# Kernel tuning notes

Hardware: AMD Instinct MI355X
Metric: run time of the kernel (lower is better)

The kernel has to match this reference:

```python
import jax, jax.numpy as jnp
import numpy as np

INTERP = 10  # gt contour interpolation factor (time=10 in source)
SMOOTH_L1_BETA = 1.0
LOSS_WEIGHT = 1.0


def interpolation(poly):
    # poly: [B, M, 2] -> [B, M*INTERP, 2]
    poly_roll = jnp.roll(poly, shift=1, axis=1)
    step = jnp.arange(INTERP, dtype=poly.dtype) / INTERP  # [INTERP]
    # [B, M, INTERP, 2]
    interp = (poly[:, :, None, :] * step[None, None, :, None]
              + poly_roll[:, :, None, :] * (1.0 - step)[None, None, :, None])
    B, M = poly.shape[0], poly.shape[1]
    return interp.reshape(B, M * INTERP, 2)


def compute_distance(pred, gt):
    # pred: [B, N, 2], gt: [B, M, 2] -> squared euclidean distance [B, M, N]
    # ||g - p||^2 = ||g||^2 + ||p||^2 - 2 g.p  (avoids materializing [B,M,N,2])
    g2 = jnp.sum(gt * gt, axis=-1)[:, :, None]    # [B, M, 1]
    p2 = jnp.sum(pred * pred, axis=-1)[:, None, :]  # [B, 1, N]
    gp = jnp.einsum('bmk,bnk->bmn', gt, pred)
    return g2 + p2 - 2.0 * gp


def smooth_l1(x, y):
    d = jnp.abs(x - y)
    return jnp.where(d < SMOOTH_L1_BETA, 0.5 * d * d / SMOOTH_L1_BETA, d - 0.5 * SMOOTH_L1_BETA)


def setup_inputs() -> dict:
    key = jax.random.key(0)
    k1, k2, k3, k4 = jax.random.split(key, 4)
    B, N, M = 1024, 128, 128
    ini_pred_poly = jax.random.normal(k1, (B, N, 2), dtype=jnp.float32)
    pred_poly = ini_pred_poly + 0.1 * jax.random.normal(k2, (B, N, 2), dtype=jnp.float32)
    gt_poly = jax.random.normal(k3, (B, M, 2), dtype=jnp.float32)
    keyPointsMask = (jax.random.uniform(k4, (B, M)) < 0.7).astype(jnp.float32)
    return {'ini_pred_poly': ini_pred_poly, 'pred_poly': pred_poly,
            'gt_poly': gt_poly, 'keyPointsMask': keyPointsMask}


def reference(ini_pred_poly, pred_poly, gt_poly, keyPointsMask):
    # --- lossPred2NearestGt ---
    gt_interp = interpolation(gt_poly)                       # [B, M*10, 2]
    d1 = compute_distance(ini_pred_poly, gt_interp)          # [B, M*10, N]
    index_gt = jnp.argmin(d1, axis=1)                        # [B, N]
    nearest_gt = jnp.take_along_axis(gt_interp, index_gt[:, :, None], axis=1)  # [B, N, 2]
    loss_pred2gt = jnp.mean(smooth_l1(pred_poly, nearest_gt))  # scalar (reduction='mean')

    # --- lossGt2NearestPred ---
    d2 = compute_distance(ini_pred_poly, gt_poly)            # [B, M, N]
    index_pred = jnp.argmin(d2, axis=2)                      # [B, M]
    nearest_pred = jnp.take_along_axis(pred_poly, index_pred[:, :, None], axis=1)  # [B, M, 2]
    loss_gt2pred = smooth_l1(nearest_pred, gt_poly)          # [B, M, 2] (reduction='none')

    # mask expanded to [B, M, 2] in the source -> its sum counts both coords
    mask = keyPointsMask[:, :, None]
    masked_sum = jnp.sum(loss_gt2pred * mask)
    mask_sum = 2.0 * jnp.sum(keyPointsMask)
    loss_set2set = masked_sum / (mask_sum + 1.0) + loss_pred2gt
    loss = loss_set2set / 2.0
    return LOSS_WEIGHT * loss
```

## Files before the change

### kernel.cpp

```cpp
#include <hip/hip_runtime.h>
#include <math.h>


#define BB 1024
#define NN 128
#define MM 128

__device__ __forceinline__ float sl1(float x) {
    float d = fabsf(x);
    return d < 1.0f ? 0.5f * d * d : d - 0.5f;
}

__global__ void __launch_bounds__(256, 8)
dmloss_main(const float* __restrict__ ini, const float* __restrict__ pred,
            const float* __restrict__ gt,  const float* __restrict__ kmask,
            float4* __restrict__ partials)
{
    const int b    = blockIdx.x >> 1;
    const int half = blockIdx.x & 1;
    const int tid  = threadIdx.x;
    const int g    = tid & 63;
    const int h    = tid >> 6;
    const int P    = (half << 6) + g;

    __shared__ __align__(16) float2 s_gt[MM];
    __shared__ float2 s_pr[NN];
    __shared__ float2 s_ii[NN];
    __shared__ float4 s_segA[MM];
    __shared__ float2 s_segB[MM];
    __shared__ float  s_step[16];
    __shared__ float  s_rv[4 * 64];
    __shared__ float  s_rf[4 * 64];
    __shared__ float  s_sum[3][4];

    const float2* gt2 = (const float2*)(gt   + (size_t)b * MM * 2);
    const float2* in2 = (const float2*)(ini  + (size_t)b * NN * 2);
    const float2* pr2 = (const float2*)(pred + (size_t)b * NN * 2);

    if (tid < 128) {
        int m = tid;
        float2 gm = gt2[m];
        float2 a  = gt2[(m + 127) & 127];
        s_gt[m] = gm;
        float ex = gm.x - a.x, ey = gm.y - a.y;
        float A  = ex * ex + ey * ey;
        float inv = A > 0.f ? 10.f / A : 0.f;
        s_segA[m] = make_float4(a.x, a.y, -ex * inv, -ey * inv);
        s_segB[m] = make_float2(ex * 0.1f, ey * 0.1f);
        if (tid < 16) s_step[tid] = (float)tid / 10.0f;
    } else {
        int k = tid - 128;
        s_pr[k] = pr2[k];
        s_ii[k] = in2[k];
    }
    float2 myP  = in2[P];
    float2 myPr = pr2[P];
    float2 myG  = gt2[P];
    float  myKm = kmask[b * MM + P];
    const float px = myP.x, py = myP.y;
    __syncthreads();

    float sumA = 0.f, sumB = 0.f, sumC = 0.f;

    float b0 = INFINITY, f0 = 1e30f;
    {
        float fm = (float)(320 * h);
        const int m0 = 32 * h;
        #pragma unroll 4
        for (int j = 0; j < 32; ++j) {
            float4 SA = s_segA[m0 + j];
            float2 SB = s_segB[m0 + j];
            float qx = SA.x - px, qy = SA.y - py;
            float jv = fmaf(qy, SA.w, qx * SA.z);
            float jr = rintf(__builtin_amdgcn_fmed3f(jv, 0.f, 9.f));
            float dx = fmaf(jr, SB.x, qx);
            float dy = fmaf(jr, SB.y, qy);
            float d  = fmaf(dy, dy, dx * dx);
            float fi = fm + jr;
            if (d < b0) { b0 = d; f0 = fi; }
            fm += 10.f;
        }
    }
    s_rv[h * 64 + g] = b0;
    s_rf[h * 64 + g] = f0;
    __syncthreads();

    if (tid < 64) {
        float best = s_rv[tid], bf = s_rf[tid];
        #pragma unroll
        for (int q = 1; q < 4; ++q) {
            float ov = s_rv[q * 64 + tid];
            float of = s_rf[q * 64 + tid];
            if (ov < best || (ov == best && of < bf)) { best = ov; bf = of; }
        }
        int bidx = (int)bf;
        int m = bidx / 10;
        int j = bidx - m * 10;
        float s  = s_step[j];
        float tt = 1.0f - s;
        float2 gm = s_gt[m];
        float2 gp = s_gt[(m + 127) & 127];
        float gx = gm.x * s + gp.x * tt;
        float gy = gm.y * s + gp.y * tt;
        float2 pr = s_pr[(half << 6) + tid];
        sumA = sl1(pr.x - gx) + sl1(pr.y - gy);
    }
    __syncthreads();

    {
        const float gx = myG.x, gy = myG.y;
        b0 = INFINITY; f0 = 1e30f;
        float fk = (float)(32 * h);
        const int k0 = 32 * h;
        #pragma unroll 4
        for (int j = 0; j < 32; ++j) {
            float2 I = s_ii[k0 + j];
            float dx = I.x - gx, dy = I.y - gy;
            float d  = fmaf(dy, dy, dx * dx);
            if (d < b0) { b0 = d; f0 = fk; }
            fk += 1.f;
        }
        s_rv[h * 64 + g] = b0;
        s_rf[h * 64 + g] = f0;
    }
    __syncthreads();

    if (tid < 64) {
        float best = s_rv[tid], bf = s_rf[tid];
        #pragma unroll
        for (int q = 1; q < 4; ++q) {
            float ov = s_rv[q * 64 + tid];
            float of = s_rf[q * 64 + tid];
            if (ov < best || (ov == best && of < bf)) { best = ov; bf = of; }
        }
        int k = (int)bf;
        float2 pk2 = s_pr[k];
        float2 g0  = s_gt[(half << 6) + tid];
        float  km  = kmask[b * MM + (half << 6) + tid];
        sumB = km * (sl1(pk2.x - g0.x) + sl1(pk2.y - g0.y));
        sumC = km;
    }

    #pragma unroll
    for (int off = 32; off > 0; off >>= 1) {
        sumA += __shfl_down(sumA, off);
        sumB += __shfl_down(sumB, off);
        sumC += __shfl_down(sumC, off);
    }
    const int wave = tid >> 6;
    if ((tid & 63) == 0) {
        s_sum[0][wave] = sumA; s_sum[1][wave] = sumB; s_sum[2][wave] = sumC;
    }
    __syncthreads();
    if (tid == 0) {
        float A = 0.f, Bs = 0.f, C = 0.f;
        #pragma unroll
        for (int w = 0; w < 4; ++w) {
            A += s_sum[0][w]; Bs += s_sum[1][w]; C += s_sum[2][w];
        }
        partials[blockIdx.x] = make_float4(A, Bs, C, 0.0f);
    }
}

__global__ void __launch_bounds__(256)
dmloss_final(const float4* __restrict__ partials, float* __restrict__ out)
{
    const int tid = threadIdx.x;
    float A = 0.0f, Bs = 0.0f, C = 0.0f;
    #pragma unroll
    for (int i = tid; i < 2 * BB; i += 256) {
        float4 p = partials[i];
        A += p.x; Bs += p.y; C += p.z;
    }
    #pragma unroll
    for (int off = 32; off > 0; off >>= 1) {
        A  += __shfl_down(A, off);
        Bs += __shfl_down(Bs, off);
        C  += __shfl_down(C, off);
    }
    __shared__ float sA[4], sB[4], sC[4];
    const int wave = tid >> 6, lane = tid & 63;
    if (lane == 0) { sA[wave] = A; sB[wave] = Bs; sC[wave] = C; }
    __syncthreads();
    if (tid == 0) {
        float a  = sA[0] + sA[1] + sA[2] + sA[3];
        float bs = sB[0] + sB[1] + sB[2] + sB[3];
        float c  = sC[0] + sC[1] + sC[2] + sC[3];
        float loss_pred2gt = a / ((float)BB * (float)NN * 2.0f);
        float loss_set2set = bs / (2.0f * c + 1.0f) + loss_pred2gt;
        out[0] = 0.5f * loss_set2set;
    }
}

extern "C" void kernel_launch(void* const* d_in, const int* in_sizes, int n_in,
                              void* d_out, int out_size, void* d_ws, size_t ws_size,
                              hipStream_t stream)
{
    const float* ini   = (const float*)d_in[0];
    const float* pred  = (const float*)d_in[1];
    const float* gt    = (const float*)d_in[2];
    const float* kmask = (const float*)d_in[3];
    float4* partials = (float4*)d_ws;

    dmloss_main<<<dim3(2 * BB), dim3(256), 0, stream>>>(ini, pred, gt, kmask, partials);
    dmloss_final<<<dim3(1), dim3(256), 0, stream>>>(partials, (float*)d_out);
}
```

Measured before the change: 18.08 us.

## Replace cross-wave argmin reduction with DPP row-rotation and per-wave role split

Each block now runs 128 threads. One wave computes the pred-to-gt nearest search and the other computes the gt-to-pred search. Query points and running (distance,index) minima are rotated across 16-lane rows with DPP row_ror, so each lane scans segments held by its row neighbours. This removes the shared-memory partial-min arrays and several block barriers. In exchange it adds per-step DPP moves and 64-bit packed compares, and halves threads per block.

```diff
diff --git a/kernel.cpp b/kernel.cpp
--- a/kernel.cpp
+++ b/kernel.cpp
@@ -6,38 +6,50 @@
 #define NN 128
 #define MM 128
 
+typedef unsigned long long u64;
+typedef unsigned int u32;
+
 __device__ __forceinline__ float sl1(float x) {
     float d = fabsf(x);
     return d < 1.0f ? 0.5f * d * d : d - 0.5f;
 }
 
-__global__ void __launch_bounds__(256, 8)
+__device__ __forceinline__ float dpp_ror1_f(float v) {
+    return __builtin_bit_cast(float,
+        __builtin_amdgcn_mov_dpp(__builtin_bit_cast(int, v), 0x121, 0xf, 0xf, false));
+}
+__device__ __forceinline__ u32 dpp_ror1_u(u32 v) {
+    return (u32)__builtin_amdgcn_mov_dpp((int)v, 0x121, 0xf, 0xf, false);
+}
+
+__global__ void __launch_bounds__(128, 8)
 dmloss_main(const float* __restrict__ ini, const float* __restrict__ pred,
             const float* __restrict__ gt,  const float* __restrict__ kmask,
             float4* __restrict__ partials)
 {
-    const int b    = blockIdx.x >> 1;
-    const int half = blockIdx.x & 1;
+    const int bid  = blockIdx.x;
+    const int b    = bid >> 1;
+    const int half = bid & 1;
     const int tid  = threadIdx.x;
-    const int g    = tid & 63;
-    const int h    = tid >> 6;
-    const int P    = (half << 6) + g;
+    const int wid  = tid >> 6;
+    const int lane = tid & 63;
+    const int lr   = lane & 15;
+    const int role = wid ^ half;
+    const int P    = (half << 6) + lane;
 
-    __shared__ __align__(16) float2 s_gt[MM];
+    __shared__ float2 s_gt[MM];
+    __shared__ float4 s_segA[MM];
+    __shared__ float2 s_segB[MM];
     __shared__ float2 s_pr[NN];
     __shared__ float2 s_ii[NN];
-    __shared__ float4 s_segA[MM];
-    __shared__ float2 s_segB[MM];
     __shared__ float  s_step[16];
-    __shared__ float  s_rv[4 * 64];
-    __shared__ float  s_rf[4 * 64];
-    __shared__ float  s_sum[3][4];
+    __shared__ float  s_sum[3][2];
 
     const float2* gt2 = (const float2*)(gt   + (size_t)b * MM * 2);
     const float2* in2 = (const float2*)(ini  + (size_t)b * NN * 2);
     const float2* pr2 = (const float2*)(pred + (size_t)b * NN * 2);
 
-    if (tid < 128) {
+    {
         int m = tid;
         float2 gm = gt2[m];
         float2 a  = gt2[(m + 127) & 127];
@@ -47,98 +59,78 @@
         float inv = A > 0.f ? 10.f / A : 0.f;
         s_segA[m] = make_float4(a.x, a.y, -ex * inv, -ey * inv);
         s_segB[m] = make_float2(ex * 0.1f, ey * 0.1f);
+        s_ii[m] = in2[m];
+        s_pr[m] = pr2[m];
         if (tid < 16) s_step[tid] = (float)tid / 10.0f;
-    } else {
-        int k = tid - 128;
-        s_pr[k] = pr2[k];
-        s_ii[k] = in2[k];
     }
     float2 myP  = in2[P];
     float2 myPr = pr2[P];
     float2 myG  = gt2[P];
     float  myKm = kmask[b * MM + P];
-    const float px = myP.x, py = myP.y;
     __syncthreads();
 
     float sumA = 0.f, sumB = 0.f, sumC = 0.f;
 
-    float b0 = INFINITY, f0 = 1e30f;
-    {
-        float fm = (float)(320 * h);
-        const int m0 = 32 * h;
-        #pragma unroll 4
-        for (int j = 0; j < 32; ++j) {
-            float4 SA = s_segA[m0 + j];
-            float2 SB = s_segB[m0 + j];
-            float qx = SA.x - px, qy = SA.y - py;
-            float jv = fmaf(qy, SA.w, qx * SA.z);
-            float jr = rintf(__builtin_amdgcn_fmed3f(jv, 0.f, 9.f));
-            float dx = fmaf(jr, SB.x, qx);
-            float dy = fmaf(jr, SB.y, qy);
-            float d  = fmaf(dy, dy, dx * dx);
-            float fi = fm + jr;
-            if (d < b0) { b0 = d; f0 = fi; }
-            fm += 10.f;
+    if (role == 0) {
+        float px = myP.x, py = myP.y;
+        u64 best = 0x7F800000FFFFFFFFull;
+        #pragma unroll 2
+        for (int g = 0; g < 8; ++g) {
+            float4 SA = s_segA[16 * g + lr];
+            float2 SB = s_segB[16 * g + lr];
+            float base = (float)(10 * (16 * g + lr));
+            #pragma unroll
+            for (int t = 0; t < 16; ++t) {
+                float qx = SA.x - px, qy = SA.y - py;
+                float jv = fmaf(qy, SA.w, qx * SA.z);
+                float jr = rintf(__builtin_amdgcn_fmed3f(jv, 0.f, 9.f));
+                float dx = fmaf(jr, SB.x, qx);
+                float dy = fmaf(jr, SB.y, qy);
+                float d  = fmaf(dy, dy, dx * dx);
+                u64 c = ((u64)__builtin_bit_cast(u32, d) << 32)
+                        | (u32)(base + jr);
+                best = c < best ? c : best;
+                px = dpp_ror1_f(px);
+                py = dpp_ror1_f(py);
+                u32 bl = dpp_ror1_u((u32)best);
+                u32 bh = dpp_ror1_u((u32)(best >> 32));
+                best = ((u64)bh << 32) | bl;
+            }
         }
-    }
-    s_rv[h * 64 + g] = b0;
-    s_rf[h * 64 + g] = f0;
-    __syncthreads();
-
-    if (tid < 64) {
-        float best = s_rv[tid], bf = s_rf[tid];
-        #pragma unroll
-        for (int q = 1; q < 4; ++q) {
-            float ov = s_rv[q * 64 + tid];
-            float of = s_rf[q * 64 + tid];
-            if (ov < best || (ov == best && of < bf)) { best = ov; bf = of; }
-        }
-        int bidx = (int)bf;
-        int m = bidx / 10;
-        int j = bidx - m * 10;
+        u32 idx = (u32)best;
+        int m = (int)idx / 10;
+        int j = (int)idx - 10 * m;
         float s  = s_step[j];
         float tt = 1.0f - s;
         float2 gm = s_gt[m];
         float2 gp = s_gt[(m + 127) & 127];
         float gx = gm.x * s + gp.x * tt;
         float gy = gm.y * s + gp.y * tt;
-        float2 pr = s_pr[(half << 6) + tid];
-        sumA = sl1(pr.x - gx) + sl1(pr.y - gy);
-    }
-    __syncthreads();
-
-    {
-        const float gx = myG.x, gy = myG.y;
-        b0 = INFINITY; f0 = 1e30f;
-        float fk = (float)(32 * h);
-        const int k0 = 32 * h;
-        #pragma unroll 4
-        for (int j = 0; j < 32; ++j) {
-            float2 I = s_ii[k0 + j];
-            float dx = I.x - gx, dy = I.y - gy;
-            float d  = fmaf(dy, dy, dx * dx);
-            if (d < b0) { b0 = d; f0 = fk; }
-            fk += 1.f;
+        sumA = sl1(myPr.x - gx) + sl1(myPr.y - gy);
+    } else {
+        float gx = myG.x, gy = myG.y;
+        u64 best = 0x7F800000FFFFFFFFull;
+        #pragma unroll 2
+        for (int g = 0; g < 8; ++g) {
+            float2 I = s_ii[16 * g + lr];
+            const u32 lo = (u32)(16 * g + lr);
+            #pragma unroll
+            for (int t = 0; t < 16; ++t) {
+                float dx = I.x - gx, dy = I.y - gy;
+                float d  = fmaf(dy, dy, dx * dx);
+                u64 c = ((u64)__builtin_bit_cast(u32, d) << 32) | lo;
+                best = c < best ? c : best;
+                gx = dpp_ror1_f(gx);
+                gy = dpp_ror1_f(gy);
+                u32 bl = dpp_ror1_u((u32)best);
+                u32 bh = dpp_ror1_u((u32)(best >> 32));
+                best = ((u64)bh << 32) | bl;
+            }
         }
-        s_rv[h * 64 + g] = b0;
-        s_rf[h * 64 + g] = f0;
-    }
-    __syncthreads();
-
-    if (tid < 64) {
-        float best = s_rv[tid], bf = s_rf[tid];
-        #pragma unroll
-        for (int q = 1; q < 4; ++q) {
-            float ov = s_rv[q * 64 + tid];
-            float of = s_rf[q * 64 + tid];
-            if (ov < best || (ov == best && of < bf)) { best = ov; bf = of; }
-        }
-        int k = (int)bf;
-        float2 pk2 = s_pr[k];
-        float2 g0  = s_gt[(half << 6) + tid];
-        float  km  = kmask[b * MM + (half << 6) + tid];
-        sumB = km * (sl1(pk2.x - g0.x) + sl1(pk2.y - g0.y));
-        sumC = km;
+        u32 k = (u32)best;
+        float2 pk = s_pr[k];
+        sumB = myKm * (sl1(pk.x - myG.x) + sl1(pk.y - myG.y));
+        sumC = myKm;
     }
 
     #pragma unroll
@@ -147,18 +139,14 @@
         sumB += __shfl_down(sumB, off);
         sumC += __shfl_down(sumC, off);
     }
-    const int wave = tid >> 6;
-    if ((tid & 63) == 0) {
-        s_sum[0][wave] = sumA; s_sum[1][wave] = sumB; s_sum[2][wave] = sumC;
+    if (lane == 0) {
+        s_sum[0][wid] = sumA; s_sum[1][wid] = sumB; s_sum[2][wid] = sumC;
     }
     __syncthreads();
     if (tid == 0) {
-        float A = 0.f, Bs = 0.f, C = 0.f;
-        #pragma unroll
-        for (int w = 0; w < 4; ++w) {
-            A += s_sum[0][w]; Bs += s_sum[1][w]; C += s_sum[2][w];
-        }
-        partials[blockIdx.x] = make_float4(A, Bs, C, 0.0f);
+        partials[bid] = make_float4(s_sum[0][0] + s_sum[0][1],
+                                    s_sum[1][0] + s_sum[1][1],
+                                    s_sum[2][0] + s_sum[2][1], 0.0f);
     }
 }
 
@@ -202,6 +190,6 @@
     const float* kmask = (const float*)d_in[3];
     float4* partials = (float4*)d_ws;
 
-    dmloss_main<<<dim3(2 * BB), dim3(256), 0, stream>>>(ini, pred, gt, kmask, partials);
+    dmloss_main<<<dim3(2 * BB), dim3(128), 0, stream>>>(ini, pred, gt, kmask, partials);
     dmloss_final<<<dim3(1), dim3(256), 0, stream>>>(partials, (float*)d_out);
 }
```

Result: slower. 24.61 us (+36.1%).
